# Optimization experiments

Measured on AMD Instinct MI355X. Metric: run time of the kernel, lower is better.

Reference implementation:

```python
import jax, jax.numpy as jnp
import numpy as np

NUM_POINTS = 72
GAMMA = 2.0
RADIUS = 15.0
W_CLS = 1.0
W_SIM = 3.0
LW_CLS = 2.0
LW_XYTL = 0.5
LW_LIOU = 2.0
K_MAX = 64
EPS = 1e-12  # F.normalize eps


def _normalize(v):
    # F.normalize over the flattened prior axis: v / max(||v||_2, eps)
    return v / jnp.maximum(jnp.linalg.norm(v), EPS)


def _liou_loss(pred, tgt):
    # pred: [..., P], tgt broadcastable; line IoU with radius, loss = 1 - iou
    lo = jnp.minimum(pred, tgt)
    hi = jnp.maximum(pred, tgt)
    ovr = (lo + RADIUS) - (hi - RADIUS)          # per-point overlap (may be < 0)
    union = (hi + RADIUS) - (lo - RADIUS)
    iou = jnp.sum(ovr, -1) / (jnp.sum(union, -1) + 1e-9)
    return 1.0 - iou


def _per_lane(feature, prior):
    # feature: [N, D] predictions for one image; prior: [D] one GT lane
    # ---- assignment cost ----
    logits = feature[:, :2]
    log_s = jax.nn.log_softmax(logits, axis=0)   # softmax over the N priors dim (dim=1 of [1,N,2])
    s = jnp.exp(log_s)
    focal_cost = jnp.sum(((1.0 - s) ** GAMMA) * log_s * prior[:2], axis=-1)  # [N]
    xy_cost = _normalize(jnp.sqrt(jnp.sum((feature[:, 3:5] - prior[3:5]) ** 2, -1)))  # [N]
    theta_cost = _normalize(feature[:, 5] - prior[5])                                  # [N]
    dis_cost = _normalize(jnp.sum(jnp.abs(feature[:, 6:] - prior[6:]), -1) / NUM_POINTS)  # [N]
    cost = W_SIM * (dis_cost * xy_cost * theta_cost) ** 2 + W_CLS * focal_cost
    # ---- dynamic top-k ----
    liou_all = _liou_loss(feature[:, 6:], prior[None, 6:])  # [N]
    k = jnp.clip(jnp.sum(liou_all).astype(jnp.int32), 1, K_MAX)
    _, idx = jax.lax.top_k(-cost, K_MAX)  # sorted ascending by cost; first k == topk(-cost, k)
    mask = (jnp.arange(K_MAX) < k).astype(feature.dtype)  # [K]
    kf = jnp.sum(mask)
    pf = feature[idx]  # [K, D] gathered predicted features
    # ---- xytl smooth-L1 on column-normalized concat([pred[:,2:6]; label[2:6]]) over valid rows ----
    rows = pf[:, 2:6]          # [K, 4]
    lab = prior[2:6]           # [4]
    colnorm = jnp.sqrt(jnp.sum((rows ** 2) * mask[:, None], 0) + lab ** 2)  # norm over the k+1 rows
    denom = jnp.maximum(colnorm, EPS)
    d = rows / denom - lab / denom  # [K, 4]
    ad = jnp.abs(d)
    sl1 = jnp.mean(jnp.where(ad < 1.0, 0.5 * d * d, ad - 0.5), -1)  # [K]
    sl1l = jnp.sum(sl1 * mask) / kf
    # ---- focal cls loss per assigned prior vs argmax of label cls ----
    tgt = jnp.argmax(prior[:2])
    lp = jax.nn.log_softmax(pf[:, :2], axis=-1)  # [K, 2]
    logpt = lp[:, tgt]
    pt = jnp.exp(logpt)
    fl_i = -((1.0 - pt) ** GAMMA) * logpt  # [K]
    fl = jnp.sum(fl_i * mask) / kf
    # ---- LIoU loss on assigned priors ----
    ll_i = _liou_loss(pf[:, 6:], prior[None, 6:])  # [K]
    ll = jnp.sum(ll_i * mask) / kf
    return sl1l, ll, fl


def setup_inputs() -> dict:
    key = jax.random.key(0)
    k1, k2 = jax.random.split(key)
    output = jax.random.normal(k1, (64, 1000, 78), dtype=jnp.float32)
    label = jax.random.normal(k2, (64, 16, 78), dtype=jnp.float32)
    return {"output": output, "label": label}


def reference(output, label):
    per_img = jax.vmap(_per_lane, in_axes=(None, 0))        # over lanes
    sl1l, ll, fl = jax.vmap(per_img, in_axes=(0, 0))(output, label)  # over batch
    sl1l = jnp.mean(sl1l)
    ll = jnp.mean(ll)
    fl = jnp.mean(fl)
    loss = (jnp.where(sl1l > 0, LW_XYTL * sl1l, 0.0)
            + jnp.where(ll > 0, LW_LIOU * ll, 0.0)
            + jnp.where(fl > 0, LW_CLS * fl, 0.0))
    return loss
```

## Files before the change

### kernel.cpp

```cpp
#include <hip/hip_runtime.h>
#include <math.h>

#define NROWS 1000
#define TWO_R_N 2160.0f
typedef unsigned int uint;
typedef unsigned long long ull;

__device__ __forceinline__ float wsumf(float v){
#pragma unroll
  for(int o=32;o;o>>=1) v += __shfl_xor(v,o,64);
  return v;
}
__device__ __forceinline__ float wmaxf(float v){
#pragma unroll
  for(int o=32;o;o>>=1) v = fmaxf(v,__shfl_xor(v,o,64));
  return v;
}

__device__ __forceinline__ void dma16(const float4* g, float4* l){
  __builtin_amdgcn_global_load_lds((const __attribute__((address_space(1))) void*)g,
                                   (__attribute__((address_space(3))) void*)l,
                                   16, 0, 0);
}

__global__ __launch_bounds__(1024,1) void clr_task(const float* __restrict__ feat,
                                                   const float* __restrict__ lab,
                                                   float* __restrict__ ws)
{
  const int b  = blockIdx.x & 63;
  const int pg = blockIdx.x >> 6;
  const float* __restrict__ F = feat + (size_t)b*NROWS*78;

  __shared__ __align__(16) float4 sBuf4[2][1280];
  __shared__ float sS[4][NROWS];
  __shared__ float sRT[4][NROWS];
  __shared__ float sC0[NROWS], sC1[NROWS];
  __shared__ float red[64];
  __shared__ int selIdx[4][64];

  const int tid=threadIdx.x, wave=tid>>6, lane=tid&63;
  const int pw = wave & 3;
  const int rg = wave >> 2;
  const int rloc16 = lane>>2, q = lane&3;

  const float* __restrict__ P = lab + ((size_t)b*16 + pg*4 + pw)*78;
  float pv[18];
#pragma unroll
  for(int s=0;s<18;++s) pv[s] = P[6+q+4*s];
  const float2* Pf2 = (const float2*)P;
  const float2 p01=Pf2[0], p23=Pf2[1], p45=Pf2[2];

  float accR=0.f, accT=0.f, accD=0.f, accL=0.f;

  {
    const float4* src4=(const float4*)F;
#pragma unroll
    for(int it=0;it<2;++it){
      int base = it*1024 + wave*64;
      if(base<=1247){
        int idx = base + lane;
        dma16(src4 + (idx>1247?1247:idx), &sBuf4[0][base]);
      }
    }
  }

  for(int c=0;c<16;++c){
    __syncthreads();
    if(c<15){
      const int limit = (c+1==15)?779:1247;
      const float4* src4=(const float4*)(F + (size_t)(c+1)*4992);
#pragma unroll
      for(int it=0;it<2;++it){
        int base = it*1024 + wave*64;
        if(base<=limit){
          int idx = base + lane;
          dma16(src4 + (idx>limit?limit:idx), &sBuf4[(c+1)&1][base]);
        }
      }
    }
    const int rows = (c<15)?64:40;
    const int rr = rg*16 + rloc16;
    if(rr<rows){
      const float* rp = (const float*)(&sBuf4[c&1][0]) + rr*78;
      float part=0.f;
#pragma unroll
      for(int s=0;s<9;++s){
        part += fabsf(rp[6+q+4*s]     - pv[s]);
        part += fabsf(rp[6+q+4*(s+9)] - pv[s+9]);
      }
      float s1 = part + __shfl_xor(part,1,64);
      float S  = s1   + __shfl_xor(s1,  2,64);
      if(q==0){
        int r = c*64 + rr;
        const float2* rp2=(const float2*)rp;
        float2 c01=rp2[0], c23=rp2[1], c45=rp2[2];
        float dr3=c23.y-p23.y, dr4=c45.x-p45.x;
        float r2=dr3*dr3+dr4*dr4;
        float tt=c45.y-p45.y;
        sS[pw][r]=S; sRT[pw][r]=sqrtf(r2)*tt;
        if(pw==0){ sC0[r]=c01.x; sC1[r]=c01.y; }
        accR+=r2; accT+=tt*tt;
        float dd=S*(1.f/72.f); accD+=dd*dd;
        accL += 1.f-(TWO_R_N-S)/(TWO_R_N+S+1e-9f);
      }
    }
  }

  {
    float vR=wsumf(accR), vT=wsumf(accT), vD=wsumf(accD), vL=wsumf(accL);
    if(lane==0){ red[wave*4]=vR; red[wave*4+1]=vT; red[wave*4+2]=vD; red[wave*4+3]=vL; }
  }
  __syncthreads();
  if (wave >= 4) return;
  const int w = wave;

  float R=0.f,T=0.f,D=0.f,L=0.f;
#pragma unroll
  for(int g=0;g<4;++g){
    int src=(4*g+w)*4;
    R+=red[src]; T+=red[src+1]; D+=red[src+2]; L+=red[src+3];
  }
  float Nr=fmaxf(sqrtf(R),1e-12f), Nt=fmaxf(sqrtf(T),1e-12f), Nd=fmaxf(sqrtf(D),1e-12f);
  const float inv = 1.f/(Nr*Nt*Nd);
  int k=(int)L; if(k<1)k=1; if(k>64)k=64;

  float m0=-INFINITY, m1=-INFINITY;
#pragma unroll
  for(int t=0;t<16;++t){ int i=t*64+lane; if(i<NROWS){ m0=fmaxf(m0,sC0[i]); m1=fmaxf(m1,sC1[i]);} }
  m0=wmaxf(m0); m1=wmaxf(m1);
  float s0=0.f, s1=0.f;
#pragma unroll
  for(int t=0;t<16;++t){ int i=t*64+lane; if(i<NROWS){ s0+=__expf(sC0[i]-m0); s1+=__expf(sC1[i]-m1);} }
  s0=wsumf(s0); s1=wsumf(s1);
  const float lse0=m0+__logf(s0), lse1=m1+__logf(s1);

  uint key[16];
  const float p0=p01.x, pp1=p01.y;
#pragma unroll
  for(int t=0;t<16;++t){
    int i=t*64+lane; uint kk=0xFFFFFFFFu;
    if(i<NROWS){
      float ls0=sC0[i]-lse0, ls1=sC1[i]-lse1;
      float e0=__expf(ls0), e1=__expf(ls1);
      float focal=(1.f-e0)*(1.f-e0)*ls0*p0 + (1.f-e1)*(1.f-e1)*ls1*pp1;
      float prod=sRT[w][i]*(sS[w][i]*(1.f/72.f))*inv;
      float cost=3.f*prod*prod+focal;
      uint x=__float_as_uint(cost);
      kk=(x&0x80000000u)?~x:(x|0x80000000u);
    }
    key[t]=kk;
  }

  uint pref=0u, r=(uint)k;
  for(int s=31;s>=0;--s){
    const uint pp=pref>>s;
    uint cnt=0u;
#pragma unroll
    for(int t=0;t<16;++t) cnt += (uint)__popcll(__ballot((key[t]>>s)==pp));
    if(r>cnt){ r-=cnt; pref|=(1u<<s); }
  }
  const uint T2=pref; uint need=r;

  const ull lmask=(1ull<<lane)-1ull;
  int base=0;
#pragma unroll
  for(int t=0;t<16;++t){
    bool lt = key[t]<T2;
    bool eq = key[t]==T2;
    ull meq=__ballot(eq);
    bool eqs = eq && ((uint)__popcll(meq&lmask)<need);
    uint teq=(uint)__popcll(meq);
    need -= (teq<need?teq:need);
    bool ssel = lt||eqs;
    ull ms=__ballot(ssel);
    if(ssel) selIdx[w][base+(int)__popcll(ms&lmask)] = t*64+lane;
    base += (int)__popcll(ms);
  }

  {
    bool act = lane<k;
    int idx = selIdx[w][act?lane:0];
    const float2* R2=(const float2*)(F+(size_t)idx*78);
    float2 g01=R2[0], g23=R2[1], g45=R2[2];
    float S = sS[w][idx];
    float mk = act?1.f:0.f;
    float n2=wsumf(g23.x*g23.x*mk), n3=wsumf(g23.y*g23.y*mk);
    float n4=wsumf(g45.x*g45.x*mk), n5=wsumf(g45.y*g45.y*mk);
    float l2=p23.x, l3=p23.y, l4=p45.x, l5=p45.y;
    float de2=fmaxf(sqrtf(n2+l2*l2),1e-12f);
    float de3=fmaxf(sqrtf(n3+l3*l3),1e-12f);
    float de4=fmaxf(sqrtf(n4+l4*l4),1e-12f);
    float de5=fmaxf(sqrtf(n5+l5*l5),1e-12f);
    float d2=g23.x/de2-l2/de2, d3=g23.y/de3-l3/de3, d4=g45.x/de4-l4/de4, d5=g45.y/de5-l5/de5;
    auto h=[](float d){ float ad=fabsf(d); return ad<1.f ? 0.5f*d*d : ad-0.5f; };
    float sl1 = 0.25f*(h(d2)+h(d3)+h(d4)+h(d5));
    float mm=fmaxf(g01.x,g01.y);
    float lsee=mm+__logf(__expf(g01.x-mm)+__expf(g01.y-mm));
    float logpt=((pp1>p0)?g01.y:g01.x)-lsee;
    float pt=__expf(logpt);
    float fl=-(1.f-pt)*(1.f-pt)*logpt;
    float ll=1.f-(TWO_R_N-S)/(TWO_R_N+S+1e-9f);
    float ssl=wsumf(sl1*mk), sll=wsumf(ll*mk), sfl=wsumf(fl*mk);
    if(lane==0){
      float invk=1.f/(float)k;
      float* o = ws + (size_t)(b*16 + pg*4 + w)*3;
      o[0]=ssl*invk; o[1]=sll*invk; o[2]=sfl*invk;
    }
  }
}

__global__ __launch_bounds__(256) void clr_finalize(const float* __restrict__ ws,
                                                    float* __restrict__ out)
{
  float a=0.f, bsum=0.f, c=0.f;
  for(int i=threadIdx.x;i<1024;i+=256){
    a    += ws[i*3+0];
    bsum += ws[i*3+1];
    c    += ws[i*3+2];
  }
  a=wsumf(a); bsum=wsumf(bsum); c=wsumf(c);
  __shared__ float r[12];
  int wave=threadIdx.x>>6, lane=threadIdx.x&63;
  if(lane==0){ r[wave*3]=a; r[wave*3+1]=bsum; r[wave*3+2]=c; }
  __syncthreads();
  if(threadIdx.x==0){
    float sa=0,sb=0,sc=0;
    for(int w2=0;w2<4;w2++){sa+=r[w2*3];sb+=r[w2*3+1];sc+=r[w2*3+2];}
    float sl1l=sa*(1.f/1024.f), ll=sb*(1.f/1024.f), fl=sc*(1.f/1024.f);
    float loss = (sl1l>0.f ? 0.5f*sl1l : 0.f)
               + (ll  >0.f ? 2.0f*ll   : 0.f)
               + (fl  >0.f ? 2.0f*fl   : 0.f);
    out[0]=loss;
  }
}

extern "C" void kernel_launch(void* const* d_in, const int* in_sizes, int n_in,
                              void* d_out, int out_size, void* d_ws, size_t ws_size,
                              hipStream_t stream)
{
  const float* feat = (const float*)d_in[0];
  const float* lab  = (const float*)d_in[1];
  float* ws  = (float*)d_ws;
  float* out = (float*)d_out;
  hipLaunchKernelGGL(clr_task, dim3(256), dim3(1024), 0, stream, feat, lab, ws);
  hipLaunchKernelGGL(clr_finalize, dim3(1), dim3(256), 0, stream, ws, out);
}
```

Baseline: 99.14 us.

## Use smaller blocks handling two lanes each with direct global row loads

The kernel drops the double-buffered global-to-LDS DMA pipeline and 1024-thread blocks. It launches 512 blocks of 256 threads, and each block handles two GT lanes at once, so every feature element loaded from global memory is compared against both lanes. Per-row side work (geometry terms, logits) is split across the quad lanes instead of being done only by q==0. This trades fewer block-wide barriers, more blocks and higher occupancy against each image being re-read by 8 blocks instead of 4, and against unstaged, uncoalesced strided global loads.

```diff
diff --git a/kernel.cpp b/kernel.cpp
--- a/kernel.cpp
+++ b/kernel.cpp
@@ -17,108 +17,94 @@
   return v;
 }
 
-__device__ __forceinline__ void dma16(const float4* g, float4* l){
-  __builtin_amdgcn_global_load_lds((const __attribute__((address_space(1))) void*)g,
-                                   (__attribute__((address_space(3))) void*)l,
-                                   16, 0, 0);
-}
-
-__global__ __launch_bounds__(1024,1) void clr_task(const float* __restrict__ feat,
-                                                   const float* __restrict__ lab,
-                                                   float* __restrict__ ws)
+__global__ __launch_bounds__(256,2) void clr_task(const float* __restrict__ feat,
+                                                  const float* __restrict__ lab,
+                                                  float* __restrict__ ws)
 {
   const int b  = blockIdx.x & 63;
   const int pg = blockIdx.x >> 6;
-  const float* __restrict__ F = feat + (size_t)b*NROWS*78;
-
-  __shared__ __align__(16) float4 sBuf4[2][1280];
-  __shared__ float sS[4][NROWS];
-  __shared__ float sRT[4][NROWS];
+  const float* __restrict__ F  = feat + (size_t)b*NROWS*78;
+  const float* __restrict__ PA = lab + ((size_t)b*16 + pg*2)*78;
+  const float* __restrict__ PB = PA + 78;
+
+  __shared__ float sS [2][NROWS];
+  __shared__ float sRT[2][NROWS];
   __shared__ float sC0[NROWS], sC1[NROWS];
-  __shared__ float red[64];
-  __shared__ int selIdx[4][64];
+  __shared__ float red[4][8];
+  __shared__ int   selIdx[2][64];
 
   const int tid=threadIdx.x, wave=tid>>6, lane=tid&63;
-  const int pw = wave & 3;
-  const int rg = wave >> 2;
-  const int rloc16 = lane>>2, q = lane&3;
-
-  const float* __restrict__ P = lab + ((size_t)b*16 + pg*4 + pw)*78;
-  float pv[18];
-#pragma unroll
-  for(int s=0;s<18;++s) pv[s] = P[6+q+4*s];
-  const float2* Pf2 = (const float2*)P;
-  const float2 p01=Pf2[0], p23=Pf2[1], p45=Pf2[2];
-
-  float accR=0.f, accT=0.f, accD=0.f, accL=0.f;
+  const int rloc16=lane>>2, q=lane&3;
+
+  float pva[18], pvb[18];
+#pragma unroll
+  for(int s=0;s<18;++s){ pva[s]=PA[6+q+4*s]; pvb[s]=PB[6+q+4*s]; }
+  const float2* PA2=(const float2*)PA;
+  const float2* PB2=(const float2*)PB;
+  const float2 a01=PA2[0], a23=PA2[1], a45=PA2[2];
+  const float2 b01=PB2[0], b23=PB2[1], b45=PB2[2];
+
+  float accR0=0.f,accT0=0.f,accD0=0.f,accL0=0.f;
+  float accR1=0.f,accT1=0.f,accD1=0.f,accL1=0.f;
+
+#pragma unroll 2
+  for(int pass=0; pass<16; ++pass){
+    const int rr = pass*64 + wave*16 + rloc16;
+    if(rr < NROWS){
+      const float* __restrict__ rp = F + rr*78;
+      float part0=0.f, part1=0.f;
+#pragma unroll
+      for(int s=0;s<9;++s){
+        const float x = rp[6+q+4*s];
+        const float y = rp[6+q+4*(s+9)];
+        part0 += fabsf(x - pva[s]);
+        part0 += fabsf(y - pva[s+9]);
+        part1 += fabsf(x - pvb[s]);
+        part1 += fabsf(y - pvb[s+9]);
+      }
+      float s1a=part0+__shfl_xor(part0,1,64);
+      float S0 = s1a +__shfl_xor(s1a, 2,64);
+      float s1b=part1+__shfl_xor(part1,1,64);
+      float S1 = s1b +__shfl_xor(s1b, 2,64);
+      if(q==0){
+        sS[0][rr]=S0; sS[1][rr]=S1;
+        float d0=S0*(1.f/72.f); accD0+=d0*d0;
+        accL0 += 1.f-(TWO_R_N-S0)/(TWO_R_N+S0+1e-9f);
+        float d1=S1*(1.f/72.f); accD1+=d1*d1;
+        accL1 += 1.f-(TWO_R_N-S1)/(TWO_R_N+S1+1e-9f);
+      } else if(q==1){
+        const float2* rp2=(const float2*)rp;
+        const float2 c23=rp2[1], c45=rp2[2];
+        float dr3=c23.y-a23.y, dr4=c45.x-a45.x, tt=c45.y-a45.y;
+        float r2=dr3*dr3+dr4*dr4;
+        sRT[0][rr]=sqrtf(r2)*tt; accR0+=r2; accT0+=tt*tt;
+        dr3=c23.y-b23.y; dr4=c45.x-b45.x; tt=c45.y-b45.y;
+        r2=dr3*dr3+dr4*dr4;
+        sRT[1][rr]=sqrtf(r2)*tt; accR1+=r2; accT1+=tt*tt;
+      } else if(q==2){
+        const float2* rp2=(const float2*)rp;
+        const float2 c01=rp2[0];
+        sC0[rr]=c01.x; sC1[rr]=c01.y;
+      }
+    }
+  }
 
   {
-    const float4* src4=(const float4*)F;
-#pragma unroll
-    for(int it=0;it<2;++it){
-      int base = it*1024 + wave*64;
-      if(base<=1247){
-        int idx = base + lane;
-        dma16(src4 + (idx>1247?1247:idx), &sBuf4[0][base]);
-      }
-    }
-  }
-
-  for(int c=0;c<16;++c){
-    __syncthreads();
-    if(c<15){
-      const int limit = (c+1==15)?779:1247;
-      const float4* src4=(const float4*)(F + (size_t)(c+1)*4992);
-#pragma unroll
-      for(int it=0;it<2;++it){
-        int base = it*1024 + wave*64;
-        if(base<=limit){
-          int idx = base + lane;
-          dma16(src4 + (idx>limit?limit:idx), &sBuf4[(c+1)&1][base]);
-        }
-      }
-    }
-    const int rows = (c<15)?64:40;
-    const int rr = rg*16 + rloc16;
-    if(rr<rows){
-      const float* rp = (const float*)(&sBuf4[c&1][0]) + rr*78;
-      float part=0.f;
-#pragma unroll
-      for(int s=0;s<9;++s){
-        part += fabsf(rp[6+q+4*s]     - pv[s]);
-        part += fabsf(rp[6+q+4*(s+9)] - pv[s+9]);
-      }
-      float s1 = part + __shfl_xor(part,1,64);
-      float S  = s1   + __shfl_xor(s1,  2,64);
-      if(q==0){
-        int r = c*64 + rr;
-        const float2* rp2=(const float2*)rp;
-        float2 c01=rp2[0], c23=rp2[1], c45=rp2[2];
-        float dr3=c23.y-p23.y, dr4=c45.x-p45.x;
-        float r2=dr3*dr3+dr4*dr4;
-        float tt=c45.y-p45.y;
-        sS[pw][r]=S; sRT[pw][r]=sqrtf(r2)*tt;
-        if(pw==0){ sC0[r]=c01.x; sC1[r]=c01.y; }
-        accR+=r2; accT+=tt*tt;
-        float dd=S*(1.f/72.f); accD+=dd*dd;
-        accL += 1.f-(TWO_R_N-S)/(TWO_R_N+S+1e-9f);
-      }
-    }
-  }
-
-  {
-    float vR=wsumf(accR), vT=wsumf(accT), vD=wsumf(accD), vL=wsumf(accL);
-    if(lane==0){ red[wave*4]=vR; red[wave*4+1]=vT; red[wave*4+2]=vD; red[wave*4+3]=vL; }
+    float vR0=wsumf(accR0), vT0=wsumf(accT0), vD0=wsumf(accD0), vL0=wsumf(accL0);
+    float vR1=wsumf(accR1), vT1=wsumf(accT1), vD1=wsumf(accD1), vL1=wsumf(accL1);
+    if(lane==0){
+      red[wave][0]=vR0; red[wave][1]=vT0; red[wave][2]=vD0; red[wave][3]=vL0;
+      red[wave][4]=vR1; red[wave][5]=vT1; red[wave][6]=vD1; red[wave][7]=vL1;
+    }
   }
   __syncthreads();
-  if (wave >= 4) return;
+  if(wave>=2) return;
   const int w = wave;
 
   float R=0.f,T=0.f,D=0.f,L=0.f;
 #pragma unroll
   for(int g=0;g<4;++g){
-    int src=(4*g+w)*4;
-    R+=red[src]; T+=red[src+1]; D+=red[src+2]; L+=red[src+3];
+    R+=red[g][4*w]; T+=red[g][4*w+1]; D+=red[g][4*w+2]; L+=red[g][4*w+3];
   }
   float Nr=fmaxf(sqrtf(R),1e-12f), Nt=fmaxf(sqrtf(T),1e-12f), Nd=fmaxf(sqrtf(D),1e-12f);
   const float inv = 1.f/(Nr*Nt*Nd);
@@ -126,13 +112,17 @@
 
   float m0=-INFINITY, m1=-INFINITY;
 #pragma unroll
-  for(int t=0;t<16;++t){ int i=t*64+lane; if(i<NROWS){ m0=fmaxf(m0,sC0[i]); m1=fmaxf(m1,sC1[i]);} }
+  for(int t=0;t<16;++t){ int i=t*64+lane; if(i<NROWS){ m0=fmaxf(m0,sC0[i]); m1=fmaxf(m1,sC1[i]); } }
   m0=wmaxf(m0); m1=wmaxf(m1);
   float s0=0.f, s1=0.f;
 #pragma unroll
-  for(int t=0;t<16;++t){ int i=t*64+lane; if(i<NROWS){ s0+=__expf(sC0[i]-m0); s1+=__expf(sC1[i]-m1);} }
+  for(int t=0;t<16;++t){ int i=t*64+lane; if(i<NROWS){ s0+=__expf(sC0[i]-m0); s1+=__expf(sC1[i]-m1); } }
   s0=wsumf(s0); s1=wsumf(s1);
   const float lse0=m0+__logf(s0), lse1=m1+__logf(s1);
+
+  const float2 p01 = w ? b01 : a01;
+  const float2 p23 = w ? b23 : a23;
+  const float2 p45 = w ? b45 : a45;
 
   uint key[16];
   const float p0=p01.x, pp1=p01.y;
@@ -203,7 +193,7 @@
     float ssl=wsumf(sl1*mk), sll=wsumf(ll*mk), sfl=wsumf(fl*mk);
     if(lane==0){
       float invk=1.f/(float)k;
-      float* o = ws + (size_t)(b*16 + pg*4 + w)*3;
+      float* o = ws + (size_t)(b*16 + pg*2 + w)*3;
       o[0]=ssl*invk; o[1]=sll*invk; o[2]=sfl*invk;
     }
   }
@@ -242,6 +232,6 @@
   const float* lab  = (const float*)d_in[1];
   float* ws  = (float*)d_ws;
   float* out = (float*)d_out;
-  hipLaunchKernelGGL(clr_task, dim3(256), dim3(1024), 0, stream, feat, lab, ws);
+  hipLaunchKernelGGL(clr_task, dim3(512), dim3(256), 0, stream, feat, lab, ws);
   hipLaunchKernelGGL(clr_finalize, dim3(1), dim3(256), 0, stream, ws, out);
 }
```

Result: no change. 97.80 us (-1.4%).
